# Kernel tuning notes

Measured on AMD Instinct MI355X. Metric: run time of the kernel, lower is better.

Reference implementation:

```python
import jax, jax.numpy as jnp
import numpy as np

D_MODEL = 1024
NUM_HEADS = 16
SCALE = 1.0 / np.sqrt(D_MODEL // NUM_HEADS)  # matches sqrt(d_model // num_heads)


def setup_inputs() -> dict:
    key = jax.random.key(0)
    ks = jax.random.split(key, 7)
    B, S, D = 4, 2048, D_MODEL
    std = 1.0 / np.sqrt(D)
    return {
        "x": jax.random.normal(ks[0], (B, S, D), dtype=jnp.float32),
        "Wq": jax.random.normal(ks[1], (D, D), dtype=jnp.float32) * std,
        "bq": jnp.zeros((D,), dtype=jnp.float32),
        "Wk": jax.random.normal(ks[2], (D, D), dtype=jnp.float32) * std,
        "bk": jnp.zeros((D,), dtype=jnp.float32),
        "Wv": jax.random.normal(ks[3], (D, D), dtype=jnp.float32) * std,
        "bv": jnp.zeros((D,), dtype=jnp.float32),
    }


def reference(x, Wq, bq, Wk, bk, Wv, bv):
    # QKV projections (nn.Linear: x @ W^T + b; here W stored as [in, out] already)
    Q = x @ Wq + bq  # [B, S, D]
    K = x @ Wk + bk
    V = x @ Wv + bv
    scores = jnp.einsum("bsd,btd->bst", Q, K) * SCALE  # [B, S, S]
    S_len = x.shape[1]
    causal = jnp.tril(jnp.ones((S_len, S_len), dtype=bool))
    scores = jnp.where(causal, scores, -jnp.inf)
    attn = jax.nn.softmax(scores, axis=-1)
    return jnp.einsum("bst,btd->bsd", attn, V)
```

## Files before the change

### kernel.cpp

```cpp
#include <hip/hip_runtime.h>
#include <hip/hip_bf16.h>
#include <cstdint>

#define D_MODEL 1024
#define SEQ     2048
#define SCALE   0.125f
#define P_ELEMS 2228224

typedef __attribute__((ext_vector_type(8))) _Float16 f16x8;
typedef __attribute__((ext_vector_type(8))) unsigned short u16x8;
typedef __attribute__((ext_vector_type(4))) float f32x4;

__device__ __forceinline__ unsigned short f2h(float f) {
  _Float16 h = (_Float16)f;
  return __builtin_bit_cast(unsigned short, h);
}
__device__ __forceinline__ float h2f(unsigned short u) {
  return (float)__builtin_bit_cast(_Float16, u);
}

__device__ __forceinline__ void gll16(const void* g, void* lds_p) {
  __builtin_amdgcn_global_load_lds(
      (const __attribute__((address_space(1))) unsigned int*)(uintptr_t)g,
      (__attribute__((address_space(3))) unsigned int*)(unsigned int)(uintptr_t)lds_p,
      16, 0, 0);
}

#define WAITV8 asm volatile("s_waitcnt vmcnt(8)" ::: "memory")
#define WAITV0 asm volatile("s_waitcnt vmcnt(0)" ::: "memory")
#define WAITL8 asm volatile("s_waitcnt lgkmcnt(8)" ::: "memory")
#define WAITL0 asm volatile("s_waitcnt lgkmcnt(0)" ::: "memory")
#define SCHEDB __builtin_amdgcn_sched_barrier(0)
#define BAR    __builtin_amdgcn_s_barrier()
#define MFMA16(a, b, c) __builtin_amdgcn_mfma_f32_16x16x32_f16(a, b, c, 0, 0, 0)

__device__ __forceinline__ void stage_tile(const unsigned short* gA, const unsigned short* gB,
                                           size_t sA, size_t sB,
                                           int k0, unsigned short* buf, int w, int lane) {
  int rl = lane >> 3;
  int sg = ((lane & 7) ^ rl) << 3;
#pragma unroll
  for (int j = 0; j < 4; j++) {
    int c = w * 4 + j;
    int row = c * 8 + rl;
    gll16(gA + (size_t)row * sA + k0 + sg, buf + c * 512);
    gll16(gB + (size_t)row * sB + k0 + sg, buf + 8192 + c * 512);
  }
}

__device__ __forceinline__ void gemm_core(const unsigned short* gA, const unsigned short* gB,
                                          size_t sA, size_t sB,
                                          unsigned short* lds0, unsigned short* lds1, int nt,
                                          int w, int lane, int wr, int wc, int l15, int l4,
                                          f32x4 acc[4][4]) {
  stage_tile(gA, gB, sA, sB, 0, lds0, w, lane);
  stage_tile(gA, gB, sA, sB, 64, lds1, w, lane);
  WAITV8; SCHEDB; BAR;
  for (int t = 0; t < nt; t++) {
    const unsigned short* buf = (t & 1) ? lds1 : lds0;
    const unsigned short* bA = buf;
    const unsigned short* bB = buf + 8192;
    f16x8 a0[4], b0[4], a1[4], b1[4];
#pragma unroll
    for (int m = 0; m < 4; m++) {
      int row = wr * 64 + m * 16 + l15, rs = row & 7;
      a0[m] = *(const f16x8*)(bA + row * 64 + ((l4 ^ rs) << 3));
    }
#pragma unroll
    for (int n = 0; n < 4; n++) {
      int row = wc * 64 + n * 16 + l15, rs = row & 7;
      b0[n] = *(const f16x8*)(bB + row * 64 + ((l4 ^ rs) << 3));
    }
#pragma unroll
    for (int m = 0; m < 4; m++) {
      int row = wr * 64 + m * 16 + l15, rs = row & 7;
      a1[m] = *(const f16x8*)(bA + row * 64 + (((4 + l4) ^ rs) << 3));
    }
#pragma unroll
    for (int n = 0; n < 4; n++) {
      int row = wc * 64 + n * 16 + l15, rs = row & 7;
      b1[n] = *(const f16x8*)(bB + row * 64 + (((4 + l4) ^ rs) << 3));
    }
    WAITL8; SCHEDB;
    __builtin_amdgcn_s_setprio(1);
#pragma unroll
    for (int m = 0; m < 4; m++)
#pragma unroll
      for (int n = 0; n < 4; n++)
        acc[m][n] = MFMA16(a0[m], b0[n], acc[m][n]);
    __builtin_amdgcn_s_setprio(0);
    WAITL0; SCHEDB; BAR;
    if (t + 2 < nt) stage_tile(gA, gB, sA, sB, (t + 2) * 64,
                               (unsigned short*)buf, w, lane);
    __builtin_amdgcn_s_setprio(1);
#pragma unroll
    for (int m = 0; m < 4; m++)
#pragma unroll
      for (int n = 0; n < 4; n++)
        acc[m][n] = MFMA16(a1[m], b1[n], acc[m][n]);
    __builtin_amdgcn_s_setprio(0);
    if (t + 2 < nt) { WAITV8; } else { WAITV0; }
    SCHEDB; BAR;
  }
}

__global__ __launch_bounds__(256) void cvt_fused(const float* __restrict__ x,
                                                 const float* __restrict__ W0,
                                                 const float* __restrict__ W1,
                                                 const float* __restrict__ W2,
                                                 unsigned short* __restrict__ xb,
                                                 unsigned short* __restrict__ wt) {
  __shared__ float t[32][33];
  int bid = blockIdx.x;
  int tid = threadIdx.x;
  if (bid < 4096) {
    int i = bid * 256 + tid;
    const float4* p = (const float4*)x + (size_t)i * 2;
    float4 a = p[0], b = p[1];
    u16x8 r;
    r[0] = f2h(a.x); r[1] = f2h(a.y); r[2] = f2h(a.z); r[3] = f2h(a.w);
    r[4] = f2h(b.x); r[5] = f2h(b.y); r[6] = f2h(b.z); r[7] = f2h(b.w);
    *((u16x8*)xb + i) = r;
  } else {
    int id = bid - 4096;
    int z = id >> 10, rem = id & 1023;
    int bx = rem & 31, by = rem >> 5;
    const float* W = (z == 0) ? W0 : (z == 1 ? W1 : W2);
    unsigned short* o = wt + (size_t)z * 1048576;
    int c0 = bx * 32, r0 = by * 32;
    int tx = tid & 31, ty = tid >> 5;
    for (int i = 0; i < 4; i++)
      t[ty + 8 * i][tx] = W[(size_t)(r0 + ty + 8 * i) * 1024 + c0 + tx];
    __syncthreads();
    for (int i = 0; i < 4; i++)
      o[(size_t)(c0 + ty + 8 * i) * 1024 + r0 + tx] = f2h(t[tx][ty + 8 * i]);
  }
}

__global__ __launch_bounds__(256) void qkv_gemm(const unsigned short* __restrict__ xb,
                                                const unsigned short* __restrict__ wt,
                                                const float* __restrict__ b0,
                                                const float* __restrict__ b1,
                                                const float* __restrict__ b2,
                                                unsigned short* __restrict__ Qp,
                                                unsigned short* __restrict__ Kp,
                                                unsigned short* __restrict__ vtp) {
  __shared__ unsigned short lds[2][16384];
  int m0 = blockIdx.x * 128;
  int n0 = blockIdx.y * 128;
  int z = n0 >> 10, nz = n0 & 1023;
  const unsigned short* gA = xb + (size_t)m0 * 1024;
  const unsigned short* gB = wt + (size_t)z * 1048576 + (size_t)nz * 1024;
  const float* bias = (z == 0) ? b0 : (z == 1 ? b1 : b2);
  int tid = threadIdx.x, lane = tid & 63, w = tid >> 6;
  int wr = w >> 1, wc = w & 1, l15 = lane & 15, l4 = lane >> 4;
  f32x4 acc[4][4] = {};
  gemm_core(gA, gB, 1024, 1024, &lds[0][0], &lds[1][0], 16, w, lane, wr, wc, l15, l4, acc);

  if (z < 2) {
    unsigned short* O = (z == 0) ? Qp : Kp;
#pragma unroll
    for (int m = 0; m < 4; m++)
#pragma unroll
      for (int n = 0; n < 4; n++) {
        int cl = wc * 64 + n * 16 + l15;
        float bv = bias[nz + cl];
#pragma unroll
        for (int r = 0; r < 4; r++) {
          int row = m0 + wr * 64 + m * 16 + l4 * 4 + r;
          O[(size_t)row * 1024 + nz + cl] = f2h(acc[m][n][r] + bv);
        }
      }
  } else {
    unsigned short* T = &lds[0][0];
#pragma unroll
    for (int m = 0; m < 4; m++)
#pragma unroll
      for (int n = 0; n < 4; n++) {
        int cl = wc * 64 + n * 16 + l15;
        float bv = bias[nz + cl];
#pragma unroll
        for (int r = 0; r < 4; r++) {
          int rl = wr * 64 + m * 16 + l4 * 4 + r;
          T[cl * 136 + rl] = f2h(acc[m][n][r] + bv);
        }
      }
    __syncthreads();
    int bidx = m0 >> 11, s0 = m0 & 2047;
#pragma unroll
    for (int i = 0; i < 8; i++) {
      int d = w * 32 + i * 4 + (lane >> 4);
      int ch = lane & 15;
      u16x8 v = *(const u16x8*)(T + d * 136 + ch * 8);
      *(u16x8*)(vtp + ((size_t)bidx * 1024 + nz + d) * 2048 + s0 + ch * 8) = v;
    }
  }
}

__global__ __launch_bounds__(256) void qk_scores(const unsigned short* __restrict__ Q,
                                                 const unsigned short* __restrict__ Kb,
                                                 unsigned short* __restrict__ sc) {
  __shared__ unsigned short lds[2][16384];
  int b = blockIdx.y;
  int i = blockIdx.x;
  int qt = (int)((sqrtf(8.f * i + 1.f) - 1.f) * 0.5f);
  while ((qt + 1) * (qt + 2) / 2 <= i) qt++;
  while (qt * (qt + 1) / 2 > i) qt--;
  int kt = i - qt * (qt + 1) / 2;
  int Wspan = (qt + 1) << 7;
  const unsigned short* gA = Q  + ((size_t)b * 2048 + qt * 128) * 1024;
  const unsigned short* gB = Kb + ((size_t)b * 2048 + kt * 128) * 1024;
  unsigned short* outp = sc + (size_t)b * P_ELEMS + (size_t)16384 * (qt * (qt + 1) / 2);
  int tid = threadIdx.x, lane = tid & 63, w = tid >> 6;
  int wr = w >> 1, wc = w & 1, l15 = lane & 15, l4 = lane >> 4;
  f32x4 acc[4][4] = {};
  gemm_core(gA, gB, 1024, 1024, &lds[0][0], &lds[1][0], 16, w, lane, wr, wc, l15, l4, acc);
#pragma unroll
  for (int m = 0; m < 4; m++)
#pragma unroll
    for (int n = 0; n < 4; n++) {
      int cl = wc * 64 + n * 16 + l15;
      int kv = kt * 128 + cl;
#pragma unroll
      for (int r = 0; r < 4; r++) {
        int rl = wr * 64 + m * 16 + l4 * 4 + r;
        int srow = qt * 128 + rl;
        float v = acc[m][n][r] * SCALE;
        if (kv > srow) v = -30000.f;
        outp[(size_t)rl * Wspan + kv] = f2h(v);
      }
    }
}

__global__ __launch_bounds__(256) void softmax_row(const unsigned short* __restrict__ sc,
                                                   unsigned short* __restrict__ pb) {
  __shared__ float redm[4];
  __shared__ float reds[4];
  int srow = blockIdx.x;
  int b = srow >> 11, sl = srow & 2047;
  int qt = sl >> 7;
  int Wspan = (qt + 1) << 7;
  size_t rb = (size_t)b * P_ELEMS + (size_t)16384 * (qt * (qt + 1) / 2) + (size_t)(sl & 127) * Wspan;
  const u16x8* src = (const u16x8*)(sc + rb);
  int nv = Wspan >> 3;
  int t = threadIdx.x, lane = t & 63, w = t >> 6;
  bool h0 = t < nv;
  float v[8];
  float mx = -1e30f;
  if (h0) {
    u16x8 raw = src[t];
#pragma unroll
    for (int j = 0; j < 8; j++) { v[j] = h2f(raw[j]); mx = fmaxf(mx, v[j]); }
  }
  for (int off = 1; off < 64; off <<= 1) mx = fmaxf(mx, __shfl_xor(mx, off, 64));
  if (lane == 0) redm[w] = mx;
  __syncthreads();
  mx = fmaxf(fmaxf(redm[0], redm[1]), fmaxf(redm[2], redm[3]));
  float s = 0.f;
  if (h0) {
#pragma unroll
    for (int j = 0; j < 8; j++) { v[j] = __expf(v[j] - mx); s += v[j]; }
  }
  for (int off = 1; off < 64; off <<= 1) s += __shfl_xor(s, off, 64);
  if (lane == 0) reds[w] = s;
  __syncthreads();
  s = reds[0] + reds[1] + reds[2] + reds[3];
  float inv = 1.f / s;
  if (h0) {
    u16x8 o;
#pragma unroll
    for (int j = 0; j < 8; j++) o[j] = f2h(v[j] * inv);
    *((u16x8*)(pb + rb) + t) = o;
  }
}

__global__ __launch_bounds__(256) void pv_gemm(const unsigned short* __restrict__ pb,
                                               const unsigned short* __restrict__ vtp,
                                               float* __restrict__ outp) {
  __shared__ unsigned short lds[2][16384];
  int p = blockIdx.x;
  int n0 = blockIdx.y * 128;
  int b = blockIdx.z;
  int tid = threadIdx.x, lane = tid & 63, w = tid >> 6;
  int wr = w >> 1, wc = w & 1, l15 = lane & 15, l4 = lane >> 4;
  const unsigned short* gB = vtp + (size_t)b * 1024 * 2048 + (size_t)n0 * 2048;
#pragma unroll
  for (int which = 0; which < 2; which++) {
    int qt = which ? (15 - p) : p;
    int Wspan = (qt + 1) << 7;
    const unsigned short* gA = pb + (size_t)b * P_ELEMS + (size_t)16384 * (qt * (qt + 1) / 2);
    float* O = outp + ((size_t)b * 2048 + qt * 128) * 1024;
    f32x4 acc[4][4] = {};
    gemm_core(gA, gB, Wspan, 2048, &lds[0][0], &lds[1][0], 2 * (qt + 1),
              w, lane, wr, wc, l15, l4, acc);
#pragma unroll
    for (int m = 0; m < 4; m++)
#pragma unroll
      for (int n = 0; n < 4; n++) {
        int cl = n0 + wc * 64 + n * 16 + l15;
#pragma unroll
        for (int r = 0; r < 4; r++) {
          int rl = wr * 64 + m * 16 + l4 * 4 + r;
          O[(size_t)rl * 1024 + cl] = acc[m][n][r];
        }
      }
  }
}

extern "C" void kernel_launch(void* const* d_in, const int* in_sizes, int n_in,
                              void* d_out, int out_size, void* d_ws, size_t ws_size,
                              hipStream_t stream) {
  const float* x  = (const float*)d_in[0];
  const float* Wq = (const float*)d_in[1];
  const float* bq = (const float*)d_in[2];
  const float* Wk = (const float*)d_in[3];
  const float* bk = (const float*)d_in[4];
  const float* Wv = (const float*)d_in[5];
  const float* bv = (const float*)d_in[6];
  float* out = (float*)d_out;

  unsigned short* ws  = (unsigned short*)d_ws;
  unsigned short* wt  = ws;
  unsigned short* Qp  = ws + 3145728;
  unsigned short* Kp  = ws + 11534336;
  unsigned short* vtp = ws + 19922944;
  unsigned short* sc  = ws + 28311552;
  unsigned short* pb  = ws + 37224448;
  unsigned short* xb  = (unsigned short*)d_out;

  cvt_fused<<<7168, 256, 0, stream>>>(x, Wq, Wk, Wv, xb, wt);
  qkv_gemm<<<dim3(64, 24), 256, 0, stream>>>(xb, wt, bq, bk, bv, Qp, Kp, vtp);
  qk_scores<<<dim3(136, 4), 256, 0, stream>>>(Qp, Kp, sc);
  softmax_row<<<8192, 256, 0, stream>>>(sc, pb);
  pv_gemm<<<dim3(8, 8, 4), 256, 0, stream>>>(pb, vtp, out);
}
```

Before: 155.3 us.

## Add 256x256-tile 8-wave GEMM kernel for Q/K projections

Adds a new qkv8 kernel that computes the Q and K projections with 256x256 tiles, 512 threads (8 waves) and a 4-phase interleaved LDS-load/MFMA schedule with staggered global prefetch. The existing 128x128 kernel now only computes V, selected through a column offset. The larger tiles are meant to raise arithmetic intensity and cut global/LDS traffic per FLOP. In exchange it needs 128KB of LDS and more accumulator registers, which may limit occupancy, and it splits the projection into two launches with 256 blocks in the first one.

```diff
diff --git a/kernel.cpp b/kernel.cpp
--- a/kernel.cpp
+++ b/kernel.cpp
@@ -27,11 +27,14 @@
 }
 
 #define WAITV8 asm volatile("s_waitcnt vmcnt(8)" ::: "memory")
+#define WAITV4 asm volatile("s_waitcnt vmcnt(4)" ::: "memory")
 #define WAITV0 asm volatile("s_waitcnt vmcnt(0)" ::: "memory")
 #define WAITL8 asm volatile("s_waitcnt lgkmcnt(8)" ::: "memory")
 #define WAITL0 asm volatile("s_waitcnt lgkmcnt(0)" ::: "memory")
 #define SCHEDB __builtin_amdgcn_sched_barrier(0)
 #define BAR    __builtin_amdgcn_s_barrier()
+#define PRIO1  __builtin_amdgcn_s_setprio(1)
+#define PRIO0  __builtin_amdgcn_s_setprio(0)
 #define MFMA16(a, b, c) __builtin_amdgcn_mfma_f32_16x16x32_f16(a, b, c, 0, 0, 0)
 
 __device__ __forceinline__ void stage_tile(const unsigned short* gA, const unsigned short* gB,
@@ -82,26 +85,157 @@
       b1[n] = *(const f16x8*)(bB + row * 64 + (((4 + l4) ^ rs) << 3));
     }
     WAITL8; SCHEDB;
-    __builtin_amdgcn_s_setprio(1);
+    PRIO1;
 #pragma unroll
     for (int m = 0; m < 4; m++)
 #pragma unroll
       for (int n = 0; n < 4; n++)
         acc[m][n] = MFMA16(a0[m], b0[n], acc[m][n]);
-    __builtin_amdgcn_s_setprio(0);
+    PRIO0;
     WAITL0; SCHEDB; BAR;
     if (t + 2 < nt) stage_tile(gA, gB, sA, sB, (t + 2) * 64,
                                (unsigned short*)buf, w, lane);
-    __builtin_amdgcn_s_setprio(1);
+    PRIO1;
 #pragma unroll
     for (int m = 0; m < 4; m++)
 #pragma unroll
       for (int n = 0; n < 4; n++)
         acc[m][n] = MFMA16(a1[m], b1[n], acc[m][n]);
-    __builtin_amdgcn_s_setprio(0);
+    PRIO0;
     if (t + 2 < nt) { WAITV8; } else { WAITV0; }
     SCHEDB; BAR;
   }
+}
+
+__device__ __forceinline__ void stage_q(const unsigned short* g, int k0,
+                                        unsigned short* dst, int w, int lane) {
+  int rl = lane >> 3;
+  int sg = ((lane & 7) ^ rl) << 3;
+#pragma unroll
+  for (int j = 0; j < 2; j++) {
+    int c = w * 2 + j;
+    int row = c * 8 + rl;
+    gll16(g + (size_t)row * 1024 + k0 + sg, dst + c * 512);
+  }
+}
+
+__global__ __launch_bounds__(512, 2) void qkv8(const unsigned short* __restrict__ xb,
+                                               const unsigned short* __restrict__ wt,
+                                               const float* __restrict__ b0f,
+                                               const float* __restrict__ b1f,
+                                               unsigned short* __restrict__ Qp,
+                                               unsigned short* __restrict__ Kp) {
+  __shared__ unsigned short lds[2][32768];
+  int m0 = blockIdx.x * 256;
+  int n0 = blockIdx.y * 256;
+  int z = n0 >> 10, nz = n0 & 1023;
+  const unsigned short* gA = xb + (size_t)m0 * 1024;
+  const unsigned short* gB = wt + (size_t)z * 1048576 + (size_t)nz * 1024;
+  const float* bias = z ? b1f : b0f;
+  unsigned short* O = z ? Kp : Qp;
+  int tid = threadIdx.x, lane = tid & 63, w = tid >> 6;
+  int wr = w >> 2, wc = w & 3, l15 = lane & 15, l4 = lane >> 4;
+  f32x4 acc[8][4] = {};
+
+  stage_q(gA,          0, &lds[0][0],     w, lane);
+  stage_q(gA + 131072, 0, &lds[0][8192],  w, lane);
+  stage_q(gB,          0, &lds[0][16384], w, lane);
+  stage_q(gB + 131072, 0, &lds[0][24576], w, lane);
+  stage_q(gA,          64, &lds[1][0],    w, lane);
+  stage_q(gA + 131072, 64, &lds[1][8192], w, lane);
+  WAITV4; SCHEDB; BAR;
+
+  f16x8 a0[4], a1[4], a2[4], a3[4], b0v[4], b1v[4];
+  for (int t = 0; t < 16; t++) {
+    unsigned short* buf = &lds[t & 1][0];
+    unsigned short* oth = &lds[(t & 1) ^ 1][0];
+    int kc1 = (t + 1) * 64, kc2 = (t + 2) * 64;
+#pragma unroll
+    for (int m = 0; m < 4; m++) {
+      int row = wr * 128 + m * 16 + l15, rs = row & 7;
+      a0[m] = *(const f16x8*)(buf + row * 64 + ((l4 ^ rs) << 3));
+    }
+#pragma unroll
+    for (int n = 0; n < 4; n++) {
+      int row = wc * 64 + n * 16 + l15, rs = row & 7;
+      b0v[n] = *(const f16x8*)(buf + 16384 + row * 64 + ((l4 ^ rs) << 3));
+    }
+    if (t + 1 < 16) stage_q(gB, kc1, oth + 16384, w, lane);
+    BAR; WAITL0; SCHEDB;
+    PRIO1;
+#pragma unroll
+    for (int m = 0; m < 4; m++)
+#pragma unroll
+      for (int n = 0; n < 4; n++)
+        acc[m][n] = MFMA16(a0[m], b0v[n], acc[m][n]);
+    PRIO0;
+    BAR;
+#pragma unroll
+    for (int m = 0; m < 4; m++) {
+      int row = wr * 128 + 64 + m * 16 + l15, rs = row & 7;
+      a1[m] = *(const f16x8*)(buf + row * 64 + ((l4 ^ rs) << 3));
+    }
+#pragma unroll
+    for (int m = 0; m < 4; m++) {
+      int row = wr * 128 + m * 16 + l15, rs = row & 7;
+      a2[m] = *(const f16x8*)(buf + row * 64 + (((4 + l4) ^ rs) << 3));
+    }
+    if (t + 1 < 16) stage_q(gB + 131072, kc1, oth + 24576, w, lane);
+    BAR; WAITL0; SCHEDB;
+    PRIO1;
+#pragma unroll
+    for (int m = 0; m < 4; m++)
+#pragma unroll
+      for (int n = 0; n < 4; n++)
+        acc[m + 4][n] = MFMA16(a1[m], b0v[n], acc[m + 4][n]);
+    PRIO0;
+    BAR;
+#pragma unroll
+    for (int m = 0; m < 4; m++) {
+      int row = wr * 128 + 64 + m * 16 + l15, rs = row & 7;
+      a3[m] = *(const f16x8*)(buf + row * 64 + (((4 + l4) ^ rs) << 3));
+    }
+#pragma unroll
+    for (int n = 0; n < 4; n++) {
+      int row = wc * 64 + n * 16 + l15, rs = row & 7;
+      b1v[n] = *(const f16x8*)(buf + 16384 + row * 64 + (((4 + l4) ^ rs) << 3));
+    }
+    BAR; WAITL0; SCHEDB;
+    PRIO1;
+#pragma unroll
+    for (int m = 0; m < 4; m++)
+#pragma unroll
+      for (int n = 0; n < 4; n++)
+        acc[m][n] = MFMA16(a2[m], b1v[n], acc[m][n]);
+    PRIO0;
+    BAR;
+    if (t + 2 < 16) {
+      stage_q(gA, kc2, buf, w, lane);
+      stage_q(gA + 131072, kc2, buf + 8192, w, lane);
+    }
+    PRIO1;
+#pragma unroll
+    for (int m = 0; m < 4; m++)
+#pragma unroll
+      for (int n = 0; n < 4; n++)
+        acc[m + 4][n] = MFMA16(a3[m], b1v[n], acc[m + 4][n]);
+    PRIO0;
+    if (t + 1 < 16) { if (t + 2 < 16) { WAITV4; } else { WAITV0; } }
+    SCHEDB; BAR;
+  }
+
+#pragma unroll
+  for (int m = 0; m < 8; m++)
+#pragma unroll
+    for (int n = 0; n < 4; n++) {
+      int cl = wc * 64 + n * 16 + l15;
+      float bv = bias[nz + cl];
+#pragma unroll
+      for (int r = 0; r < 4; r++) {
+        int row = m0 + wr * 128 + m * 16 + l4 * 4 + r;
+        O[(size_t)row * 1024 + nz + cl] = f2h(acc[m][n][r] + bv);
+      }
+    }
 }
 
 __global__ __launch_bounds__(256) void cvt_fused(const float* __restrict__ x,
@@ -144,10 +278,11 @@
                                                 const float* __restrict__ b2,
                                                 unsigned short* __restrict__ Qp,
                                                 unsigned short* __restrict__ Kp,
-                                                unsigned short* __restrict__ vtp) {
+                                                unsigned short* __restrict__ vtp,
+                                                int n_off) {
   __shared__ unsigned short lds[2][16384];
   int m0 = blockIdx.x * 128;
-  int n0 = blockIdx.y * 128;
+  int n0 = n_off + blockIdx.y * 128;
   int z = n0 >> 10, nz = n0 & 1023;
   const unsigned short* gA = xb + (size_t)m0 * 1024;
   const unsigned short* gB = wt + (size_t)z * 1048576 + (size_t)nz * 1024;
@@ -329,7 +464,8 @@
   unsigned short* xb  = (unsigned short*)d_out;
 
   cvt_fused<<<7168, 256, 0, stream>>>(x, Wq, Wk, Wv, xb, wt);
-  qkv_gemm<<<dim3(64, 24), 256, 0, stream>>>(xb, wt, bq, bk, bv, Qp, Kp, vtp);
+  qkv8<<<dim3(32, 8), 512, 0, stream>>>(xb, wt, bq, bk, Qp, Kp);
+  qkv_gemm<<<dim3(64, 8), 256, 0, stream>>>(xb, wt, bq, bk, bv, Qp, Kp, vtp, 2048);
   qk_scores<<<dim3(136, 4), 256, 0, stream>>>(Qp, Kp, sc);
   softmax_row<<<8192, 256, 0, stream>>>(sc, pb);
   pv_gemm<<<dim3(8, 8, 4), 256, 0, stream>>>(pb, vtp, out);
```

After: 156.3 us. No clear change (+0.6%).
